# Kernel optimization log

Hardware: AMD Instinct MI355X
Metric: run time of the kernel (lower is better)

Reference implementation:

```python
import jax, jax.numpy as jnp
import numpy as np

SIGMA = 1.0
KSIZE = 5
WEAK = 75.0
STRONG = 255.0
LOW_T = 0.00392
HIGH_T = 0.15

# scipy.signal.gaussian(M, std): unnormalized gaussian window
_n = np.arange(KSIZE, dtype=np.float32) - (KSIZE - 1) / 2.0
_g = np.exp(-0.5 * (_n / SIGMA) ** 2).astype(np.float32)
GAUSS_H = jnp.asarray(_g.reshape(1, 1, 1, KSIZE))  # horizontal 1xK
GAUSS_V = jnp.asarray(_g.reshape(1, 1, KSIZE, 1))  # vertical Kx1

_sobel = np.array([[1, 0, -1], [2, 0, -2], [1, 0, -1]], dtype=np.float32)
SOBEL_H = jnp.asarray(_sobel.reshape(1, 1, 3, 3))
SOBEL_V = jnp.asarray(_sobel.T.reshape(1, 1, 3, 3))

_f0 = np.array([[0, 0, 0], [0, 1, -1], [0, 0, 0]], np.float32)
_f45 = np.array([[0, 0, 0], [0, 1, 0], [0, 0, -1]], np.float32)
_f90 = np.array([[0, 0, 0], [0, 1, 0], [0, -1, 0]], np.float32)
_f135 = np.array([[0, 0, 0], [0, 1, 0], [-1, 0, 0]], np.float32)
_f180 = np.array([[0, 0, 0], [-1, 1, 0], [0, 0, 0]], np.float32)
_f225 = np.array([[-1, 0, 0], [0, 1, 0], [0, 0, 0]], np.float32)
_f270 = np.array([[0, -1, 0], [0, 1, 0], [0, 0, 0]], np.float32)
_f315 = np.array([[0, 0, -1], [0, 1, 0], [0, 0, 0]], np.float32)
DIR_FILT = jnp.asarray(np.stack([_f0, _f45, _f90, _f135, _f180, _f225, _f270, _f315]).reshape(8, 1, 3, 3))

NBR_FILT = jnp.asarray(np.array([[1, 1, 1], [1, 0, 1], [1, 1, 1]], np.float32).reshape(1, 1, 3, 3))


def _conv(x, w, pad):
    # cross-correlation, matching torch F.conv2d
    return jax.lax.conv_general_dilated(
        x, w, window_strides=(1, 1), padding=[(pad[0], pad[0]), (pad[1], pad[1])],
        dimension_numbers=('NCHW', 'OIHW', 'NCHW'))


def setup_inputs() -> dict:
    key = jax.random.key(0)
    img = jax.random.uniform(key, (16, 1, 1024, 1024), dtype=jnp.float32)
    return {"img": img}


def reference(img):
    B = img.shape[0]
    # --- gaussian noise removal (separable) ---
    sm = _conv(img, GAUSS_H, (0, KSIZE // 2))
    sm = _conv(sm, GAUSS_V, (KSIZE // 2, 0))
    # --- sobel gradients ---
    Ix = _conv(sm, SOBEL_H, (1, 1))
    Iy = _conv(sm, SOBEL_V, (1, 1))
    mag = jnp.sqrt(Ix ** 2 + Iy ** 2)
    mag = mag / mag.reshape(B, -1).max(axis=1).reshape(B, 1, 1, 1)
    direction = jnp.arctan2(Iy, Ix) * (180.0 / 3.1415926) + 180.0
    direction = jnp.round(direction / 45.0) * 45.0
    # --- non-max suppression via directional differences + gather ---
    all_filtered = _conv(mag, DIR_FILT, (1, 1))  # [B,8,H,W]
    idx_pos = (direction / 45.0).astype(jnp.int32) % 8  # [B,1,H,W]
    idx_neg = (idx_pos + 4) % 8
    cs_pos = jnp.take_along_axis(all_filtered, idx_pos, axis=1)
    cs_neg = jnp.take_along_axis(all_filtered, idx_neg, axis=1)
    is_max = jnp.minimum(cs_pos, cs_neg) > 0.0
    thin = jnp.where(is_max, mag, 0.0)
    # --- double threshold ---
    hi = thin.max() * HIGH_T  # global max, as in source
    strong = thin >= hi
    weak = (thin < hi) & (thin >= LOW_T)
    inter = jnp.where(strong, STRONG, jnp.where(weak, WEAK, 0.0))
    # --- hysteresis: iterate until no weak pixel gains a strong neighbor ---
    def cond(state):
        return state[1]

    def body(state):
        x, _ = state
        weak_m = x == WEAK
        sn = _conv((x == STRONG).astype(jnp.float32), NBR_FILT, (1, 1))
        new_strong = weak_m & (sn > 0.0)
        x = jnp.where(new_strong, STRONG, x)
        return x, new_strong.any()

    final, _ = jax.lax.while_loop(cond, body, (inter, jnp.asarray(True)))
    final = jnp.where(final == STRONG, final, 0.0)
    return final
```

## Files before the change

### kernel.cpp

```cpp
#include <hip/hip_runtime.h>
#include <math.h>

#define BB 16
#define H 1024
#define W 1024
#define HW (H*W)
#define NTOT (BB*HW)
#define CAP 262144u

typedef unsigned long long u64;

__device__ __constant__ float GW[5] = {
    0.13533528323661270f, 0.60653065971263342f, 1.0f,
    0.60653065971263342f, 0.13533528323661270f};

__device__ __constant__ int NBDY[8] = {0, 1, 1, 1, 0, -1, -1, -1};
__device__ __constant__ int NBDX[8] = {1, 1, 0, -1, -1, -1, 0, 1};

#define CSCALE ((float)(180.0 / 3.1415926))

__global__ __launch_bounds__(256, 6) void k_smooth_sobel_nms(
    const float* __restrict__ img, float* __restrict__ thin,
    float* __restrict__ partialA, float* __restrict__ partialB,
    unsigned int* __restrict__ cnt, uint4* __restrict__ list) {
#pragma clang fp contract(off)
    __shared__ float sA[24 * 80];
    __shared__ float sB[24 * 76];
    unsigned short* sBk = (unsigned short*)&sA[1600];
    float* redS = &sA[1800];

    const int tid = threadIdx.x;
    const int x0 = blockIdx.x * 64;
    const int y0 = blockIdx.y * 16;
    const int b = blockIdx.z;
    const size_t base = (size_t)b * HW;

    for (int idx = tid; idx < 24 * 20; idx += 256) {
        int r = idx / 20, v = idx - r * 20;
        int gy = y0 - 4 + r;
        int gxv = x0 - 8 + v * 4;
        float4 val = make_float4(0.f, 0.f, 0.f, 0.f);
        if (gy >= 0 && gy < H && gxv >= 0 && gxv <= W - 4)
            val = *(const float4*)&img[base + (size_t)gy * W + gxv];
        *(float4*)&sA[r * 80 + v * 4] = val;
    }
    __syncthreads();

    for (int idx = tid; idx < 24 * 19; idx += 256) {
        int r = idx / 19, g = idx - r * 19;
        const float* p = &sA[r * 80 + g * 4];
        float4 A0 = *(const float4*)p;
        float4 A1 = *(const float4*)(p + 4);
        float a_[8] = {A0.x, A0.y, A0.z, A0.w, A1.x, A1.y, A1.z, A1.w};
        float o[4];
#pragma unroll
        for (int j = 0; j < 4; ++j) {
            float s = 0.0f;
#pragma unroll
            for (int k = 0; k < 5; ++k) s = s + GW[k] * a_[j + k];
            o[j] = s;
        }
        *(float4*)&sB[r * 76 + g * 4] = make_float4(o[0], o[1], o[2], o[3]);
    }
    __syncthreads();

    for (int idx = tid; idx < 20 * 19; idx += 256) {
        int rr = idx / 19, g = idx - rr * 19;
        float bb[20];
#pragma unroll
        for (int k = 0; k < 5; ++k) {
            float4 t = *(const float4*)&sB[(rr + k) * 76 + g * 4];
            bb[k * 4 + 0] = t.x; bb[k * 4 + 1] = t.y;
            bb[k * 4 + 2] = t.z; bb[k * 4 + 3] = t.w;
        }
        int gy = y0 - 2 + rr;
        bool rowok = (gy >= 0 && gy < H);
        float o[4];
#pragma unroll
        for (int j = 0; j < 4; ++j) {
            float s = 0.0f;
#pragma unroll
            for (int k = 0; k < 5; ++k) s = s + GW[k] * bb[k * 4 + j];
            int gx = x0 - 6 + g * 4 + j;
            o[j] = (rowok && gx >= 0 && gx < W) ? s : 0.0f;
        }
        *(float4*)&sA[rr * 80 + g * 4] = make_float4(o[0], o[1], o[2], o[3]);
    }
    __syncthreads();

    for (int idx = tid; idx < 18 * 18; idx += 256) {
        int m = idx / 18, gq = idx - m * 18;
        const float* P0 = &sA[m * 80 + gq * 4];
        const float* P1 = P0 + 80;
        const float* P2 = P1 + 80;
        float4 q0 = *(const float4*)P0; float4 e0 = *(const float4*)(P0 + 4);
        float4 q1 = *(const float4*)P1; float4 e1 = *(const float4*)(P1 + 4);
        float4 q2 = *(const float4*)P2; float4 e2 = *(const float4*)(P2 + 4);
        float r0[8] = {q0.x, q0.y, q0.z, q0.w, e0.x, e0.y, e0.z, e0.w};
        float r1[8] = {q1.x, q1.y, q1.z, q1.w, e1.x, e1.y, e1.z, e1.w};
        float r2[8] = {q2.x, q2.y, q2.z, q2.w, e2.x, e2.y, e2.z, e2.w};
        int gy = y0 - 1 + m;
        unsigned int bk = 0;
        float mg[4];
#pragma unroll
        for (int j = 0; j < 4; ++j) {
            float a00 = r0[j + 1], a01 = r0[j + 2], a02 = r0[j + 3];
            float a10 = r1[j + 1],                  a12 = r1[j + 3];
            float a20 = r2[j + 1], a21 = r2[j + 2], a22 = r2[j + 3];

            float Ix = a00;
            Ix = Ix - a02;
            Ix = Ix + 2.0f * a10;
            Ix = Ix - 2.0f * a12;
            Ix = Ix + a20;
            Ix = Ix - a22;

            float Iy = a00;
            Iy = Iy + 2.0f * a01;
            Iy = Iy + a02;
            Iy = Iy - a20;
            Iy = Iy - 2.0f * a21;
            Iy = Iy - a22;

            float t1 = Ix * Ix;
            float t2 = Iy * Iy;
            float m2 = sqrtf(t1 + t2);
            int gx = x0 - 4 + gq * 4 + j;
            if (gy < 0 || gy >= H || gx < 0 || gx >= W) m2 = 0.0f;
            mg[j] = m2;

            float ax = fabsf(Ix), ay = fabsf(Iy);
            float mn = fminf(ax, ay), mx = fmaxf(ax, ay);
            float cr = mn * 0.92387953f - mx * 0.38268343f;
            int bidx;
            if (fabsf(cr) < mx * 3e-5f) {
                float fa2 = (float)atan2((double)Iy, (double)Ix);
                float d2 = fa2 * CSCALE;
                d2 = d2 + 180.0f;
                float t2d = d2 / 45.0f;
                float rr2 = rintf(t2d);
                bidx = ((int)rr2) & 7;
            } else if (ay <= ax * 0.41421356f) {
                bidx = signbit(Ix) ? 0 : 4;
            } else if (ay >= ax * 2.41421356f) {
                bidx = (Iy >= 0.0f) ? 6 : 2;
            } else {
                bidx = (Iy >= 0.0f) ? ((Ix >= 0.0f) ? 5 : 7)
                                    : ((Ix >= 0.0f) ? 3 : 1);
            }
            bk |= ((unsigned int)bidx) << (4 * j);
        }
        *(float4*)&sB[m * 76 + gq * 4] = make_float4(mg[0], mg[1], mg[2], mg[3]);
        sBk[m * 18 + gq] = (unsigned short)bk;
    }
    __syncthreads();

    const int r = tid >> 4;
    const int cg = (tid & 15) * 4;
    const int y = y0 + r;
    const int m = r + 1;
    float tmax = 0.0f, amax = 0.0f;
    {
        unsigned int bk4 = sBk[m * 18 + (cg >> 2) + 1];
        float4 a4 = *(const float4*)&sB[m * 76 + cg + 4];
        float av[4] = {a4.x, a4.y, a4.z, a4.w};
        float o[4];
#pragma unroll
        for (int j = 0; j < 4; ++j) {
            int bkt = (bk4 >> (4 * j)) & 7;
            int dy = NBDY[bkt], dx = NBDX[bkt];
            int cm = cg + 4 + j;
            float a = av[j];
            float bp = sB[(m + dy) * 76 + cm + dx];
            float bn = sB[(m - dy) * 76 + cm - dx];
            bool g1 = a > bp, g2 = a > bn;
            bool im = g1 && g2;
            if (im) {
                bool f1 = a >= bp * 1.0000005f;
                bool f2 = a >= bn * 1.0000005f;
                if (!(f1 && f2)) {
                    im = false;
                    unsigned int id = atomicAdd(cnt, 1u);
                    if (id < CAP) {
                        uint4 e;
                        e.x = (unsigned int)(base + (size_t)y * W + x0 + cg + j);
                        e.y = __float_as_uint(a);
                        e.z = __float_as_uint(bp);
                        e.w = __float_as_uint(bn);
                        list[id] = e;
                    }
                }
            }
            tmax = fmaxf(tmax, a);
            if (im) amax = fmaxf(amax, a);
            o[j] = im ? a : 0.0f;
        }
        *(float4*)&thin[base + (size_t)y * W + x0 + cg] =
            make_float4(o[0], o[1], o[2], o[3]);
    }
#pragma unroll
    for (int off = 32; off > 0; off >>= 1) {
        tmax = fmaxf(tmax, __shfl_down(tmax, off));
        amax = fmaxf(amax, __shfl_down(amax, off));
    }
    if ((tid & 63) == 0) { redS[tid >> 6] = tmax; redS[4 + (tid >> 6)] = amax; }
    __syncthreads();
    if (tid == 0) {
        float tA = fmaxf(fmaxf(redS[0], redS[1]), fmaxf(redS[2], redS[3]));
        float tB = fmaxf(fmaxf(redS[4], redS[5]), fmaxf(redS[6], redS[7]));
        int pb = (b * 64 + blockIdx.y) * 16 + blockIdx.x;
        partialA[pb] = tA;
        partialB[pb] = tB;
    }
}

__global__ __launch_bounds__(1024) void k_post(const float* __restrict__ partialA,
                                               const float* __restrict__ partialB,
                                               const unsigned int* __restrict__ cnt,
                                               const uint4* __restrict__ list,
                                               float* __restrict__ thin,
                                               float* __restrict__ hdr,
                                               float* __restrict__ thr) {
#pragma clang fp contract(off)
    __shared__ float sM[16];
    __shared__ int sAmaxI[16];
    __shared__ float sTm[16];
    __shared__ float sTmAll;
    const int tid = threadIdx.x;
    const int iw = tid >> 6, lane = tid & 63;

    {
        const float* p = partialA + iw * 1024;
        float m = 0.0f;
        for (int k = lane; k < 1024; k += 64) m = fmaxf(m, p[k]);
        for (int off = 32; off > 0; off >>= 1) m = fmaxf(m, __shfl_down(m, off));
        if (lane == 0) { sM[iw] = m; sAmaxI[iw] = 0; hdr[iw] = m; }
    }
    __syncthreads();

    {
        unsigned int n = *cnt;
        if (n > CAP) n = CAP;
        for (unsigned int i = tid; i < n; i += 1024) {
            uint4 e = list[i];
            float a = __uint_as_float(e.y);
            float bp = __uint_as_float(e.z);
            float bn = __uint_as_float(e.w);
            int b = (int)(e.x >> 20);
            float M = sM[b];
            bool f1 = a >= bp * 1.0000005f;
            bool f2 = a >= bn * 1.0000005f;
            float qa = a / M;
            bool r1 = f1 ? true : (qa > (bp / M));
            bool r2 = f2 ? true : (qa > (bn / M));
            if (r1 && r2) {
                thin[e.x] = a;
                atomicMax(&sAmaxI[b], __float_as_int(a));
            }
        }
    }
    __syncthreads();

    {
        const float* p = partialB + iw * 1024;
        float m = 0.0f;
        for (int k = lane; k < 1024; k += 64) m = fmaxf(m, p[k]);
        for (int off = 32; off > 0; off >>= 1) m = fmaxf(m, __shfl_down(m, off));
        if (lane == 0) {
            m = fmaxf(m, __int_as_float(sAmaxI[iw]));
            sTm[iw] = m / sM[iw];
        }
    }
    __syncthreads();
    if (tid == 0) {
        float tm = 0.0f;
        for (int i = 0; i < 16; ++i) tm = fmaxf(tm, sTm[i]);
        hdr[16] = tm;
        sTmAll = tm;
    }
    __syncthreads();
    if (tid < 32) {
        float tm = sTmAll;
        int t = tid;
        float M = sM[t >> 1];
        float T = (t & 1) ? (tm * 0.15f) : 0.00392f;
        if (0.0f / M >= T) { thr[t] = 0.0f; return; }
        unsigned int lo = 0u, hi = 0x7f800000u;
        while (hi - lo > 1u) {
            unsigned int mid = lo + ((hi - lo) >> 1);
            if (__uint_as_float(mid) / M >= T) hi = mid; else lo = mid;
        }
        thr[t] = __uint_as_float(hi);
    }
}

__global__ __launch_bounds__(256, 8) void k_thresh_b(const float* __restrict__ thin,
                                                     const float* __restrict__ hdr,
                                                     const float* __restrict__ thr,
                                                     u64* __restrict__ Sb,
                                                     u64* __restrict__ Wb) {
    __shared__ unsigned int nibS[256], nibW[256];
    const int tid = threadIdx.x;
    const int x0 = blockIdx.x * 128;
    const int y0 = blockIdx.y * 32;
    const int b = blockIdx.z;
    const size_t base = (size_t)b * HW;
    const float Alo = thr[b * 2], Ahi = thr[b * 2 + 1];
    const bool snm = (hdr[16] * 0.15f <= 0.0f);
    const int r = tid >> 5;
    const int cg = (tid & 31) * 4;

    for (int k4 = 0; k4 < 4; ++k4) {
        const int rr = k4 * 8 + r;
        const int y = y0 + rr;
        float4 a4 = *(const float4*)&thin[base + (size_t)y * W + x0 + cg];
        float av[4] = {a4.x, a4.y, a4.z, a4.w};
        unsigned int ns = 0, nw = 0;
#pragma unroll
        for (int j = 0; j < 4; ++j) {
            bool strong = snm || (av[j] >= Ahi);
            bool weak = (!strong) && (av[j] >= Alo);
            ns |= (strong ? 1u : 0u) << j;
            nw |= (weak ? 1u : 0u) << j;
        }
        nibS[tid] = ns;
        nibW[tid] = nw;
        __syncthreads();
        if (tid < 32) {
            bool isW = (tid >= 16);
            int t = tid & 15;
            int rw = t >> 1, h = t & 1;
            const unsigned int* nb = isW ? nibW : nibS;
            u64 w = 0;
#pragma unroll
            for (int j = 0; j < 16; ++j)
                w |= (u64)nb[rw * 32 + h * 16 + j] << (4 * j);
            int yy = y0 + k4 * 8 + rw;
            int widx2 = ((b << 8) | ((yy >> 6) << 4) | ((x0 >> 6) + h)) * 64 + (yy & 63);
            if (isW) Wb[widx2] = w; else Sb[widx2] = w;
        }
        __syncthreads();
    }
}

template <bool LAST>
__global__ __launch_bounds__(256) void k_hyster_bits(const u64* __restrict__ Wb,
                                                     u64* __restrict__ Sb,
                                                     float* __restrict__ out) {
    const int lane = threadIdx.x & 63;
    const int t = blockIdx.x * 4 + (threadIdx.x >> 6);
    const int ty = (t >> 4) & 15;
    const int tx = t & 15;
    const int idx = t * 64 + lane;

    u64 S = Sb[idx];
    const u64 Wk = Wb[idx];

    u64 hstat = 0;
    if (tx > 0)  hstat |= (Sb[(t - 1) * 64 + lane] >> 63) & 1ull;
    if (tx < 15) hstat |= (Sb[(t + 1) * 64 + lane] & 1ull) << 63;

    u64 halo = 0;
    if (lane == 0 && ty > 0) {
        const int ta = t - 16;
        u64 tc = Sb[ta * 64 + 63];
        u64 hh = (tc << 1) | tc | (tc >> 1);
        if (tx > 0)  hh |= (Sb[(ta - 1) * 64 + 63] >> 63) & 1ull;
        if (tx < 15) hh |= (Sb[(ta + 1) * 64 + 63] & 1ull) << 63;
        halo = hh;
    }
    if (lane == 63 && ty < 15) {
        const int tb = t + 16;
        u64 tc = Sb[tb * 64 + 0];
        u64 hh = (tc << 1) | tc | (tc >> 1);
        if (tx > 0)  hh |= (Sb[(tb - 1) * 64 + 0] >> 63) & 1ull;
        if (tx < 15) hh |= (Sb[(tb + 1) * 64 + 0] & 1ull) << 63;
        halo = hh;
    }

    for (int it = 0; it < 160; ++it) {
        u64 hh = (S << 1) | S | (S >> 1) | hstat;
        u64 up = __shfl_up(hh, 1, 64);
        if (lane == 0) up = halo;
        u64 dn = __shfl_down(hh, 1, 64);
        if (lane == 63) dn = halo;
        u64 dil = hh | up | dn;
        u64 nS = S | (Wk & dil);
        bool ch = (nS != S);
        S = nS;
        if (!__any(ch)) break;
    }

    if (!LAST) {
        Sb[idx] = S;
    } else {
        const int bimg = t >> 8;
        float* op = out + (size_t)bimg * HW + (size_t)(ty * 64) * W + tx * 64 + lane;
#pragma unroll 4
        for (int rr = 0; rr < 64; ++rr) {
            u64 wrow = __shfl(S, rr, 64);
            op[(size_t)rr * W] = ((wrow >> lane) & 1ull) ? 255.0f : 0.0f;
        }
    }
}

extern "C" void kernel_launch(void* const* d_in, const int* in_sizes, int n_in,
                              void* d_out, int out_size, void* d_ws, size_t ws_size,
                              hipStream_t stream) {
    (void)in_sizes; (void)n_in; (void)out_size; (void)ws_size;
    const float* img = (const float*)d_in[0];
    float* out = (float*)d_out;

    float* hdr = (float*)d_ws;
    float* thr = hdr + 64;
    unsigned int* cnt = (unsigned int*)(hdr + 96);
    float* partialA = hdr + 128;
    float* partialB = partialA + 16384;
    uint4* list = (uint4*)(partialB + 16384);
    float* thin = (float*)((char*)list + (size_t)CAP * 16);
    u64* Sb = (u64*)(thin + (size_t)NTOT);
    u64* Wb = Sb + NTOT / 64;

    hipMemsetAsync(cnt, 0, sizeof(unsigned int), stream);

    dim3 blk(256);
    k_smooth_sobel_nms<<<dim3(16, 64, BB), blk, 0, stream>>>(img, thin, partialA,
                                                             partialB, cnt, list);
    k_post<<<dim3(1), dim3(1024), 0, stream>>>(partialA, partialB, cnt, list,
                                               thin, hdr, thr);
    k_thresh_b<<<dim3(8, 32, BB), blk, 0, stream>>>(thin, hdr, thr, Sb, Wb);
    for (int p = 0; p < 5; ++p)
        k_hyster_bits<false><<<dim3(NTOT / (64 * 64) / 4), blk, 0, stream>>>(Wb, Sb, out);
    k_hyster_bits<true><<<dim3(NTOT / (64 * 64) / 4), blk, 0, stream>>>(Wb, Sb, out);
}
```

Measured before the change: 258.4 us.

## Pad shared-memory row stride and use in-row run propagation in hysteresis

Changes the shared tile row stride from 80 to 84 floats so the strided float4 accesses in the smoothing/Sobel stages hit fewer LDS bank conflicts, and moves the other scratch arrays to match. In the tile-local hysteresis loop, each iteration now fills strong pixels along whole connected runs of weak pixels within a 64-bit row using log-step masked shifts, instead of growing one pixel per iteration. The static halo and hstat contributions are applied once before the loop. This is meant to cut the number of shuffle iterations needed to converge, in exchange for more ALU work per iteration.

```diff
diff --git a/kernel.cpp b/kernel.cpp
--- a/kernel.cpp
+++ b/kernel.cpp
@@ -24,10 +24,10 @@
     float* __restrict__ partialA, float* __restrict__ partialB,
     unsigned int* __restrict__ cnt, uint4* __restrict__ list) {
 #pragma clang fp contract(off)
-    __shared__ float sA[24 * 80];
+    __shared__ float sA[2200];
     __shared__ float sB[24 * 76];
-    unsigned short* sBk = (unsigned short*)&sA[1600];
-    float* redS = &sA[1800];
+    unsigned short* sBk = (unsigned short*)&sA[2016];
+    float* redS = &sA[2178];
 
     const int tid = threadIdx.x;
     const int x0 = blockIdx.x * 64;
@@ -42,13 +42,13 @@
         float4 val = make_float4(0.f, 0.f, 0.f, 0.f);
         if (gy >= 0 && gy < H && gxv >= 0 && gxv <= W - 4)
             val = *(const float4*)&img[base + (size_t)gy * W + gxv];
-        *(float4*)&sA[r * 80 + v * 4] = val;
+        *(float4*)&sA[r * 84 + v * 4] = val;
     }
     __syncthreads();
 
     for (int idx = tid; idx < 24 * 19; idx += 256) {
         int r = idx / 19, g = idx - r * 19;
-        const float* p = &sA[r * 80 + g * 4];
+        const float* p = &sA[r * 84 + g * 4];
         float4 A0 = *(const float4*)p;
         float4 A1 = *(const float4*)(p + 4);
         float a_[8] = {A0.x, A0.y, A0.z, A0.w, A1.x, A1.y, A1.z, A1.w};
@@ -84,15 +84,15 @@
             int gx = x0 - 6 + g * 4 + j;
             o[j] = (rowok && gx >= 0 && gx < W) ? s : 0.0f;
         }
-        *(float4*)&sA[rr * 80 + g * 4] = make_float4(o[0], o[1], o[2], o[3]);
+        *(float4*)&sA[rr * 84 + g * 4] = make_float4(o[0], o[1], o[2], o[3]);
     }
     __syncthreads();
 
     for (int idx = tid; idx < 18 * 18; idx += 256) {
         int m = idx / 18, gq = idx - m * 18;
-        const float* P0 = &sA[m * 80 + gq * 4];
-        const float* P1 = P0 + 80;
-        const float* P2 = P1 + 80;
+        const float* P0 = &sA[m * 84 + gq * 4];
+        const float* P1 = P0 + 84;
+        const float* P2 = P1 + 84;
         float4 q0 = *(const float4*)P0; float4 e0 = *(const float4*)(P0 + 4);
         float4 q1 = *(const float4*)P1; float4 e1 = *(const float4*)(P1 + 4);
         float4 q2 = *(const float4*)P2; float4 e2 = *(const float4*)(P2 + 4);
@@ -378,14 +378,35 @@
         halo = hh;
     }
 
+    {
+        u64 eu = __shfl_up(hstat, 1, 64);
+        u64 ed = __shfl_down(hstat, 1, 64);
+        if (lane == 0)  eu = halo;
+        if (lane == 63) ed = halo;
+        S |= Wk & (hstat | eu | ed);
+    }
+
     for (int it = 0; it < 160; ++it) {
-        u64 hh = (S << 1) | S | (S >> 1) | hstat;
+        u64 x = S;
+        x |= (x << 1) & Wk;
+        x |= (x >> 1) & Wk;
+        u64 pL = Wk & (Wk << 1);
+        u64 pR = Wk & (Wk >> 1);
+        x |= (x << 2) & pL;   x |= (x >> 2) & pR;
+        pL &= pL << 2;        pR &= pR >> 2;
+        x |= (x << 4) & pL;   x |= (x >> 4) & pR;
+        pL &= pL << 4;        pR &= pR >> 4;
+        x |= (x << 8) & pL;   x |= (x >> 8) & pR;
+        pL &= pL << 8;        pR &= pR >> 8;
+        x |= (x << 16) & pL;  x |= (x >> 16) & pR;
+        pL &= pL << 16;       pR &= pR >> 16;
+        x |= (x << 32) & pL;  x |= (x >> 32) & pR;
+        u64 hh = x | (x << 1) | (x >> 1);
         u64 up = __shfl_up(hh, 1, 64);
-        if (lane == 0) up = halo;
+        if (lane == 0) up = 0;
         u64 dn = __shfl_down(hh, 1, 64);
-        if (lane == 63) dn = halo;
-        u64 dil = hh | up | dn;
-        u64 nS = S | (Wk & dil);
+        if (lane == 63) dn = 0;
+        u64 nS = x | (Wk & (up | dn));
         bool ch = (nS != S);
         S = nS;
         if (!__any(ch)) break;
```

New measurement: 262.3 us. About the same (+1.5%).
